# Performance work log

Hardware: AMD Instinct MI355X
Metric: run time of the kernel (lower is better)

Reference implementation:

```python
import jax, jax.numpy as jnp
import numpy as np

LN_EPS = 1e-5


def setup_inputs() -> dict:
    key = jax.random.key(0)
    k_seq, k_fc, k_mlp = jax.random.split(key, 3)
    seq = jax.random.normal(k_seq, (1408, 256), dtype=jnp.float32)
    ln_g = jnp.ones((256,), dtype=jnp.float32)
    ln_b = jnp.zeros((256,), dtype=jnp.float32)
    # kaiming-uniform-ish init scale for Linear weights
    fc_w = jax.random.uniform(k_fc, (128, 256), dtype=jnp.float32, minval=-1.0, maxval=1.0) / np.sqrt(256)
    fc_b = jnp.zeros((128,), dtype=jnp.float32)
    mlp_w = jax.random.uniform(k_mlp, (10, 128), dtype=jnp.float32, minval=-1.0, maxval=1.0) / np.sqrt(128)
    mlp_b = jnp.zeros((10,), dtype=jnp.float32)
    return {"seq": seq, "ln_g": ln_g, "ln_b": ln_b, "fc_w": fc_w,
            "fc_b": fc_b, "mlp_w": mlp_w, "mlp_b": mlp_b}


def reference(seq, ln_g, ln_b, fc_w, fc_b, mlp_w, mlp_b):
    # hardcoded reshape as in the original module
    x = seq.reshape(32, 4, 11, 256)
    # LayerNorm over last dim (256), eps=1e-5
    mu = jnp.mean(x, axis=-1, keepdims=True)
    var = jnp.mean(jnp.square(x - mu), axis=-1, keepdims=True)
    x = (x - mu) * jax.lax.rsqrt(var + LN_EPS) * ln_g + ln_b
    # Linear(256 -> 128) + Sigmoid
    h = jax.nn.sigmoid(jnp.einsum('bthd,fd->bthf', x, fc_w) + fc_b)
    # Linear(128 -> nb_classes)
    out = jnp.einsum('bthf,cf->bthc', h, mlp_w) + mlp_b
    return out
```

## Files before the change

kernel.cpp:

```cpp
#include <hip/hip_runtime.h>
#include <hip/hip_bf16.h>

#define D   256
#define F   128
#define C   10
#define LN_EPS 1e-5f

typedef __attribute__((ext_vector_type(8))) short short8;
typedef __attribute__((ext_vector_type(4))) short short4v;
typedef __attribute__((ext_vector_type(4))) float f32x4;

__device__ __forceinline__ short f2bf(float f) {
    __hip_bfloat16 h = __float2bfloat16(f);
    return *reinterpret_cast<short*>(&h);
}
__device__ __forceinline__ short8 pack8(float4 a, float4 b) {
    short8 r;
    r[0] = f2bf(a.x); r[1] = f2bf(a.y); r[2] = f2bf(a.z); r[3] = f2bf(a.w);
    r[4] = f2bf(b.x); r[5] = f2bf(b.y); r[6] = f2bf(b.z); r[7] = f2bf(b.w);
    return r;
}

__global__ __launch_bounds__(256, 1) void logreg_fused(
    const float* __restrict__ seq,   const float* __restrict__ ln_g,
    const float* __restrict__ ln_b,  const float* __restrict__ fc_w,
    const float* __restrict__ fc_b,  const float* __restrict__ mlp_w,
    const float* __restrict__ mlp_b, float* __restrict__ out)
{
    __shared__ short sxb[16 * D];
    __shared__ float sh[8][F];

    const int t    = threadIdx.x;
    const int w    = t >> 6;
    const int lane = t & 63;
    const int q    = lane >> 4;
    const int col  = lane & 15;
    const int rowbase = blockIdx.x * 8;
    const int obase   = 32 * w;

    float4 v0 = ((const float4*)(seq + (size_t)(rowbase + 2 * w)     * D))[lane];
    float4 v1 = ((const float4*)(seq + (size_t)(rowbase + 2 * w + 1) * D))[lane];
    const float4 gv = ((const float4*)ln_g)[lane];
    const float4 bv = ((const float4*)ln_b)[lane];

    float4 wf[2][16];
    #pragma unroll
    for (int ts = 0; ts < 2; ++ts) {
        const float4* __restrict__ wr =
            (const float4*)fc_w + (size_t)(obase + 16 * ts + col) * (D / 4) + 2 * q;
        #pragma unroll
        for (int kk = 0; kk < 8; ++kk) {
            wf[ts][2 * kk]     = wr[8 * kk];
            wf[ts][2 * kk + 1] = wr[8 * kk + 1];
        }
    }
    float fcb0 = fc_b[obase + col];
    float fcb1 = fc_b[obase + 16 + col];

    {
        float s0 = v0.x + v0.y + v0.z + v0.w;
        float q0 = v0.x * v0.x + v0.y * v0.y + v0.z * v0.z + v0.w * v0.w;
        float s1 = v1.x + v1.y + v1.z + v1.w;
        float q1 = v1.x * v1.x + v1.y * v1.y + v1.z * v1.z + v1.w * v1.w;
        #pragma unroll
        for (int off = 32; off > 0; off >>= 1) {
            s0 += __shfl_xor(s0, off);  q0 += __shfl_xor(q0, off);
            s1 += __shfl_xor(s1, off);  q1 += __shfl_xor(q1, off);
        }
        const float m0 = s0 * (1.0f / D), m1 = s1 * (1.0f / D);
        const float i0 = rsqrtf(q0 * (1.0f / D) - m0 * m0 + LN_EPS);
        const float i1 = rsqrtf(q1 * (1.0f / D) - m1 * m1 + LN_EPS);
        float4 o0, o1;
        o0.x = (v0.x - m0) * i0 * gv.x + bv.x;  o1.x = (v1.x - m1) * i1 * gv.x + bv.x;
        o0.y = (v0.y - m0) * i0 * gv.y + bv.y;  o1.y = (v1.y - m1) * i1 * gv.y + bv.y;
        o0.z = (v0.z - m0) * i0 * gv.z + bv.z;  o1.z = (v1.z - m1) * i1 * gv.z + bv.z;
        o0.w = (v0.w - m0) * i0 * gv.w + bv.w;  o1.w = (v1.w - m1) * i1 * gv.w + bv.w;

        short4v a0, a1;
        a0[0] = f2bf(o0.x); a0[1] = f2bf(o0.y); a0[2] = f2bf(o0.z); a0[3] = f2bf(o0.w);
        a1[0] = f2bf(o1.x); a1[1] = f2bf(o1.y); a1[2] = f2bf(o1.z); a1[3] = f2bf(o1.w);
        const int r0 = 2 * w, r1 = 2 * w + 1;
        *(short4v*)((char*)sxb + (((r0 * 512) + lane * 8) ^ (r0 << 4))) = a0;
        *(short4v*)((char*)sxb + (((r1 * 512) + lane * 8) ^ (r1 << 4))) = a1;
    }

    short8 wb0[8], wb1[8];
    #pragma unroll
    for (int kk = 0; kk < 8; ++kk) {
        wb0[kk] = pack8(wf[0][2 * kk], wf[0][2 * kk + 1]);
        wb1[kk] = pack8(wf[1][2 * kk], wf[1][2 * kk + 1]);
    }

    asm volatile("s_waitcnt lgkmcnt(0)" ::: "memory");
    __builtin_amdgcn_s_barrier();

    float w2a[C], w2b[C], mb[C];
    #pragma unroll
    for (int c = 0; c < C; ++c) {
        w2a[c] = mlp_w[c * F + lane];
        w2b[c] = mlp_w[c * F + lane + 64];
        mb[c]  = mlp_b[c];
    }

    f32x4 acc0 = {0.f, 0.f, 0.f, 0.f};
    f32x4 acc1 = {0.f, 0.f, 0.f, 0.f};
    #pragma unroll
    for (int kk = 0; kk < 8; ++kk) {
        const int boff = ((col * 512) + kk * 64 + q * 16) ^ (col << 4);
        short8 a = *(const short8*)((const char*)sxb + boff);
        acc0 = __builtin_amdgcn_mfma_f32_16x16x32_bf16(a, wb0[kk], acc0, 0, 0, 0);
        acc1 = __builtin_amdgcn_mfma_f32_16x16x32_bf16(a, wb1[kk], acc1, 0, 0, 0);
    }

    if (lane < 32) {
        #pragma unroll
        for (int rg = 0; rg < 4; ++rg) {
            const int r = q * 4 + rg;
            sh[r][obase + col]      = 1.0f / (1.0f + __expf(-(acc0[rg] + fcb0)));
            sh[r][obase + 16 + col] = 1.0f / (1.0f + __expf(-(acc1[rg] + fcb1)));
        }
    }

    asm volatile("s_waitcnt lgkmcnt(0)" ::: "memory");
    __builtin_amdgcn_s_barrier();

    {
        const int r0 = 2 * w, r1 = 2 * w + 1;
        const float h0a = sh[r0][lane], h0b = sh[r0][lane + 64];
        const float h1a = sh[r1][lane], h1b = sh[r1][lane + 64];
        #pragma unroll
        for (int c = 0; c < C; ++c) {
            float p0 = h0a * w2a[c] + h0b * w2b[c];
            float p1 = h1a * w2a[c] + h1b * w2b[c];
            #pragma unroll
            for (int off = 32; off > 0; off >>= 1) {
                p0 += __shfl_xor(p0, off);
                p1 += __shfl_xor(p1, off);
            }
            if (lane == 0) {
                out[(size_t)(rowbase + r0) * C + c] = p0 + mb[c];
                out[(size_t)(rowbase + r1) * C + c] = p1 + mb[c];
            }
        }
    }
}

extern "C" void kernel_launch(void* const* d_in, const int* in_sizes, int n_in,
                              void* d_out, int out_size, void* d_ws, size_t ws_size,
                              hipStream_t stream)
{
    const float* seq   = (const float*)d_in[0];
    const float* ln_g  = (const float*)d_in[1];
    const float* ln_b  = (const float*)d_in[2];
    const float* fc_w  = (const float*)d_in[3];
    const float* fc_b  = (const float*)d_in[4];
    const float* mlp_w = (const float*)d_in[5];
    const float* mlp_b = (const float*)d_in[6];
    float* out = (float*)d_out;

    logreg_fused<<<176, 256, 0, stream>>>(seq, ln_g, ln_b, fc_w, fc_b,
                                          mlp_w, mlp_b, out);
}
```

Baseline: 13.16 us.

## Process 16 rows per block and compute second linear with bf16 MFMA

Each block now handles 16 rows instead of 8, so every MFMA tile is fully used and the grid drops from 176 to 88 blocks. The sigmoid outputs are written as bf16 into swizzled shared memory, and the 128->10 projection runs as a 16x16x32 bf16 MFMA instead of per-class wave shuffle reductions. The aim is to cut shuffle-reduction latency and halve the per-row cost of loading and converting fc_w. In exchange the hidden activations are rounded to bf16, only 88 CUs are busy, and three of the four waves compute the final MFMA redundantly.

```diff
diff --git a/kernel.cpp b/kernel.cpp
--- a/kernel.cpp
+++ b/kernel.cpp
@@ -28,18 +28,20 @@
     const float* __restrict__ mlp_b, float* __restrict__ out)
 {
     __shared__ short sxb[16 * D];
-    __shared__ float sh[8][F];
+    __shared__ short shb[16 * F];
 
     const int t    = threadIdx.x;
     const int w    = t >> 6;
     const int lane = t & 63;
     const int q    = lane >> 4;
     const int col  = lane & 15;
-    const int rowbase = blockIdx.x * 8;
+    const int rowbase = blockIdx.x * 16;
     const int obase   = 32 * w;
 
-    float4 v0 = ((const float4*)(seq + (size_t)(rowbase + 2 * w)     * D))[lane];
-    float4 v1 = ((const float4*)(seq + (size_t)(rowbase + 2 * w + 1) * D))[lane];
+    float4 v0 = ((const float4*)(seq + (size_t)(rowbase + 4 * w)     * D))[lane];
+    float4 v1 = ((const float4*)(seq + (size_t)(rowbase + 4 * w + 1) * D))[lane];
+    float4 v2 = ((const float4*)(seq + (size_t)(rowbase + 4 * w + 2) * D))[lane];
+    float4 v3 = ((const float4*)(seq + (size_t)(rowbase + 4 * w + 3) * D))[lane];
     const float4 gv = ((const float4*)ln_g)[lane];
     const float4 bv = ((const float4*)ln_b)[lane];
 
@@ -54,53 +56,62 @@
             wf[ts][2 * kk + 1] = wr[8 * kk + 1];
         }
     }
-    float fcb0 = fc_b[obase + col];
-    float fcb1 = fc_b[obase + 16 + col];
+    float4 wf2[8] = {};
+    if (col < C) {
+        const float4* __restrict__ wr2 = (const float4*)(mlp_w + (size_t)col * F) + 2 * q;
+        #pragma unroll
+        for (int kk = 0; kk < 4; ++kk) {
+            wf2[2 * kk]     = wr2[8 * kk];
+            wf2[2 * kk + 1] = wr2[8 * kk + 1];
+        }
+    }
+    const float mbv  = (col < C) ? mlp_b[col] : 0.0f;
+    const float fcb0 = fc_b[obase + col];
+    const float fcb1 = fc_b[obase + 16 + col];
 
     {
-        float s0 = v0.x + v0.y + v0.z + v0.w;
-        float q0 = v0.x * v0.x + v0.y * v0.y + v0.z * v0.z + v0.w * v0.w;
-        float s1 = v1.x + v1.y + v1.z + v1.w;
-        float q1 = v1.x * v1.x + v1.y * v1.y + v1.z * v1.z + v1.w * v1.w;
+        float4 vv[4] = {v0, v1, v2, v3};
+        float s[4], qq[4];
+        #pragma unroll
+        for (int rr = 0; rr < 4; ++rr) {
+            s[rr]  = vv[rr].x + vv[rr].y + vv[rr].z + vv[rr].w;
+            qq[rr] = vv[rr].x * vv[rr].x + vv[rr].y * vv[rr].y
+                   + vv[rr].z * vv[rr].z + vv[rr].w * vv[rr].w;
+        }
         #pragma unroll
         for (int off = 32; off > 0; off >>= 1) {
-            s0 += __shfl_xor(s0, off);  q0 += __shfl_xor(q0, off);
-            s1 += __shfl_xor(s1, off);  q1 += __shfl_xor(q1, off);
+            #pragma unroll
+            for (int rr = 0; rr < 4; ++rr) {
+                s[rr]  += __shfl_xor(s[rr],  off);
+                qq[rr] += __shfl_xor(qq[rr], off);
+            }
         }
-        const float m0 = s0 * (1.0f / D), m1 = s1 * (1.0f / D);
-        const float i0 = rsqrtf(q0 * (1.0f / D) - m0 * m0 + LN_EPS);
-        const float i1 = rsqrtf(q1 * (1.0f / D) - m1 * m1 + LN_EPS);
-        float4 o0, o1;
-        o0.x = (v0.x - m0) * i0 * gv.x + bv.x;  o1.x = (v1.x - m1) * i1 * gv.x + bv.x;
-        o0.y = (v0.y - m0) * i0 * gv.y + bv.y;  o1.y = (v1.y - m1) * i1 * gv.y + bv.y;
-        o0.z = (v0.z - m0) * i0 * gv.z + bv.z;  o1.z = (v1.z - m1) * i1 * gv.z + bv.z;
-        o0.w = (v0.w - m0) * i0 * gv.w + bv.w;  o1.w = (v1.w - m1) * i1 * gv.w + bv.w;
-
-        short4v a0, a1;
-        a0[0] = f2bf(o0.x); a0[1] = f2bf(o0.y); a0[2] = f2bf(o0.z); a0[3] = f2bf(o0.w);
-        a1[0] = f2bf(o1.x); a1[1] = f2bf(o1.y); a1[2] = f2bf(o1.z); a1[3] = f2bf(o1.w);
-        const int r0 = 2 * w, r1 = 2 * w + 1;
-        *(short4v*)((char*)sxb + (((r0 * 512) + lane * 8) ^ (r0 << 4))) = a0;
-        *(short4v*)((char*)sxb + (((r1 * 512) + lane * 8) ^ (r1 << 4))) = a1;
+        #pragma unroll
+        for (int rr = 0; rr < 4; ++rr) {
+            const int r = 4 * w + rr;
+            const float m  = s[rr] * (1.0f / D);
+            const float iv = rsqrtf(qq[rr] * (1.0f / D) - m * m + LN_EPS);
+            short4v a;
+            a[0] = f2bf((vv[rr].x - m) * iv * gv.x + bv.x);
+            a[1] = f2bf((vv[rr].y - m) * iv * gv.y + bv.y);
+            a[2] = f2bf((vv[rr].z - m) * iv * gv.z + bv.z);
+            a[3] = f2bf((vv[rr].w - m) * iv * gv.w + bv.w);
+            *(short4v*)((char*)sxb + (((r * 512) + lane * 8) ^ (r << 4))) = a;
+        }
     }
 
-    short8 wb0[8], wb1[8];
+    short8 wb0[8], wb1[8], wb2[4];
     #pragma unroll
     for (int kk = 0; kk < 8; ++kk) {
         wb0[kk] = pack8(wf[0][2 * kk], wf[0][2 * kk + 1]);
         wb1[kk] = pack8(wf[1][2 * kk], wf[1][2 * kk + 1]);
     }
+    #pragma unroll
+    for (int kk = 0; kk < 4; ++kk)
+        wb2[kk] = pack8(wf2[2 * kk], wf2[2 * kk + 1]);
 
     asm volatile("s_waitcnt lgkmcnt(0)" ::: "memory");
     __builtin_amdgcn_s_barrier();
-
-    float w2a[C], w2b[C], mb[C];
-    #pragma unroll
-    for (int c = 0; c < C; ++c) {
-        w2a[c] = mlp_w[c * F + lane];
-        w2b[c] = mlp_w[c * F + lane + 64];
-        mb[c]  = mlp_b[c];
-    }
 
     f32x4 acc0 = {0.f, 0.f, 0.f, 0.f};
     f32x4 acc1 = {0.f, 0.f, 0.f, 0.f};
@@ -112,34 +123,31 @@
         acc1 = __builtin_amdgcn_mfma_f32_16x16x32_bf16(a, wb1[kk], acc1, 0, 0, 0);
     }
 
-    if (lane < 32) {
-        #pragma unroll
-        for (int rg = 0; rg < 4; ++rg) {
-            const int r = q * 4 + rg;
-            sh[r][obase + col]      = 1.0f / (1.0f + __expf(-(acc0[rg] + fcb0)));
-            sh[r][obase + 16 + col] = 1.0f / (1.0f + __expf(-(acc1[rg] + fcb1)));
-        }
+    #pragma unroll
+    for (int rg = 0; rg < 4; ++rg) {
+        const int r  = q * 4 + rg;
+        const float h0 = 1.0f / (1.0f + __expf(-(acc0[rg] + fcb0)));
+        const float h1 = 1.0f / (1.0f + __expf(-(acc1[rg] + fcb1)));
+        *(short*)((char*)shb + ((r * 256 + 2 * (obase + col))      ^ ((r & 7) << 4))) = f2bf(h0);
+        *(short*)((char*)shb + ((r * 256 + 2 * (obase + 16 + col)) ^ ((r & 7) << 4))) = f2bf(h1);
     }
 
     asm volatile("s_waitcnt lgkmcnt(0)" ::: "memory");
     __builtin_amdgcn_s_barrier();
 
     {
-        const int r0 = 2 * w, r1 = 2 * w + 1;
-        const float h0a = sh[r0][lane], h0b = sh[r0][lane + 64];
-        const float h1a = sh[r1][lane], h1b = sh[r1][lane + 64];
+        f32x4 acc2 = {0.f, 0.f, 0.f, 0.f};
         #pragma unroll
-        for (int c = 0; c < C; ++c) {
-            float p0 = h0a * w2a[c] + h0b * w2b[c];
-            float p1 = h1a * w2a[c] + h1b * w2b[c];
+        for (int kk = 0; kk < 4; ++kk) {
+            const int boff = (col * 256 + kk * 64 + q * 16) ^ ((col & 7) << 4);
+            short8 a = *(const short8*)((const char*)shb + boff);
+            acc2 = __builtin_amdgcn_mfma_f32_16x16x32_bf16(a, wb2[kk], acc2, 0, 0, 0);
+        }
+        if (w == 0 && col < C) {
             #pragma unroll
-            for (int off = 32; off > 0; off >>= 1) {
-                p0 += __shfl_xor(p0, off);
-                p1 += __shfl_xor(p1, off);
-            }
-            if (lane == 0) {
-                out[(size_t)(rowbase + r0) * C + c] = p0 + mb[c];
-                out[(size_t)(rowbase + r1) * C + c] = p1 + mb[c];
+            for (int rg = 0; rg < 4; ++rg) {
+                const int r = q * 4 + rg;
+                out[(size_t)(rowbase + r) * C + col] = acc2[rg] + mbv;
             }
         }
     }
@@ -158,6 +166,6 @@
     const float* mlp_b = (const float*)d_in[6];
     float* out = (float*)d_out;
 
-    logreg_fused<<<176, 256, 0, stream>>>(seq, ln_g, ln_b, fc_w, fc_b,
-                                          mlp_w, mlp_b, out);
+    logreg_fused<<<88, 256, 0, stream>>>(seq, ln_g, ln_b, fc_w, fc_b,
+                                         mlp_w, mlp_b, out);
 }
```

Result: no change. 12.91 us (-1.9%).
